# Performance work log

Hardware: AMD Instinct MI355X
Metric: run time of the kernel (lower is better)

Reference implementation:

```python
import jax, jax.numpy as jnp
import numpy as np

N = 50000   # nodes
E = 1600000 # edges
D = 128     # feature dim (in = hidden = 128)


def setup_inputs() -> dict:
    key = jax.random.key(0)
    k1, k2, k3, k4 = jax.random.split(key, 4)
    scale = 1.0 / np.sqrt(D)
    return {
        "x": jax.random.normal(k1, (N, D), jnp.float32),
        "edge_index": jax.random.randint(k2, (2, E), 0, N, dtype=jnp.int32),
        "W0": jax.random.normal(k3, (D, D), jnp.float32) * scale,
        "b0": jnp.zeros((D,), jnp.float32),
        "W1": jax.random.normal(k4, (D, D), jnp.float32) * scale,
        "b1": jnp.zeros((D,), jnp.float32),
    }


def _gcn_norm(edge_index, num_nodes):
    # Add self-loops, compute symmetric normalization D^-1/2 A_hat D^-1/2.
    loop = jnp.arange(num_nodes, dtype=edge_index.dtype)
    src = jnp.concatenate([edge_index[0], loop])
    dst = jnp.concatenate([edge_index[1], loop])
    deg = jax.ops.segment_sum(jnp.ones_like(dst, jnp.float32), dst,
                              num_segments=num_nodes)
    dinv = jnp.where(deg > 0, jax.lax.rsqrt(deg), 0.0)
    norm = dinv[dst] * dinv[src]  # [E+N]
    return src, dst, norm


def _gcn_layer(x, src, dst, norm, W, b, num_nodes):
    h = x @ W                                  # [N, D]
    msg = h[src] * norm[:, None]               # gather + scale  [E+N, D]
    out = jax.ops.segment_sum(msg, dst, num_segments=num_nodes)  # scatter-add
    return out + b


def reference(x, edge_index, W0, b0, W1, b1):
    num_nodes = x.shape[0]
    src, dst, norm = _gcn_norm(edge_index, num_nodes)
    # forward loops over the first k=2 convs, ReLU after each (as in source)
    x = jax.nn.relu(_gcn_layer(x, src, dst, norm, W0, b0, num_nodes))
    x = jax.nn.relu(_gcn_layer(x, src, dst, norm, W1, b1, num_nodes))
    return x
```

## Files before the change

kernel.cpp:

```cpp
#include <hip/hip_runtime.h>
#include <hip/hip_bf16.h>

#define D 128
#define CHUNK 8192


typedef __attribute__((ext_vector_type(8))) short short8;
typedef __attribute__((ext_vector_type(4))) float floatx4;

static __device__ inline unsigned int f2bf(float f) {
    unsigned int u = __float_as_uint(f);
    return (u + 0x7FFFu + ((u >> 16) & 1u)) >> 16;
}
static __device__ inline float bflo(unsigned int u) { return __uint_as_float(u << 16); }
static __device__ inline float bfhi(unsigned int u) { return __uint_as_float(u & 0xFFFF0000u); }

__global__ __launch_bounds__(256) void k01_swz_hist(const float* __restrict__ W0,
                                                    const float* __restrict__ W1,
                                                    short8* __restrict__ whi0, short8* __restrict__ wlo0,
                                                    short8* __restrict__ whi1, short8* __restrict__ wlo1,
                                                    const int* __restrict__ dst,
                                                    int* __restrict__ blockhist, int E_) {
    __shared__ int h[256];
    const int tid = threadIdx.x;
    if (blockIdx.x < 16) {
        int gid = blockIdx.x * 256 + tid;
        const float* W = (gid < 2048) ? W0 : W1;
        short8* whi = (gid < 2048) ? whi0 : whi1;
        short8* wlo = (gid < 2048) ? wlo0 : wlo1;
        int t2 = gid & 2047;
        int t = t2 >> 8, q = (t2 >> 6) & 3, lane = t2 & 63;
        short8 hi, lo;
        #pragma unroll
        for (int j = 0; j < 8; ++j) {
            int k = q * 32 + (lane >> 4) * 8 + j;
            int n = t * 16 + (lane & 15);
            float w = W[k * D + n];
            unsigned int hh = f2bf(w);
            hi[j] = (short)hh;
            lo[j] = (short)f2bf(w - __uint_as_float(hh << 16));
        }
        whi[t2] = hi;
        wlo[t2] = lo;
    } else {
        const int b = blockIdx.x - 16;
        h[tid] = 0;
        __syncthreads();
        const int e0 = b * CHUNK;
        const int e1 = min(E_, e0 + CHUNK);
        for (int e = e0 + tid; e < e1; e += 256)
            atomicAdd(&h[dst[e] >> 8], 1);
        __syncthreads();
        blockhist[b * 256 + tid] = h[tid];
    }
}

__global__ __launch_bounds__(256) void k2_scan(const int* __restrict__ blockhist,
                                               int* __restrict__ gbase,
                                               int* __restrict__ bucket_offs,
                                               int NB, int NBUK, int E_) {
    __shared__ int s[256];
    const int myb = blockIdx.x, tid = threadIdx.x;
    int total = 0, prefix = 0;
    #pragma unroll 4
    for (int b2 = 0; b2 < NB; ++b2) {
        int t = blockhist[b2 * 256 + tid];
        total += t;
        prefix += (b2 < myb) ? t : 0;
    }
    s[tid] = total;
    __syncthreads();
    #pragma unroll
    for (int off = 1; off < 256; off <<= 1) {
        int x = (tid >= off) ? s[tid - off] : 0;
        __syncthreads();
        s[tid] += x;
        __syncthreads();
    }
    int bstart = s[tid] - total;
    gbase[myb * 256 + tid] = bstart + prefix;
    if (myb == 0) {
        if (tid < NBUK) bucket_offs[tid] = bstart;
        if (tid == 0) bucket_offs[NBUK] = E_;
    }
}

__global__ __launch_bounds__(256) void k3_scatter(const int* __restrict__ dst,
                                                  const int* __restrict__ src,
                                                  const int* __restrict__ gbase,
                                                  unsigned int* __restrict__ buf, int E_) {
    __shared__ int c[256];
    const int b = blockIdx.x, tid = threadIdx.x;
    c[tid] = gbase[b * 256 + tid];
    __syncthreads();
    const int e0 = b * CHUNK;
    const int e1 = min(E_, e0 + CHUNK);
    for (int e = e0 + tid; e < e1; e += 256) {
        int v = dst[e];
        int sdx = src[e];
        int pos = atomicAdd(&c[v >> 8], 1);
        buf[pos] = (unsigned int)sdx | ((unsigned int)(v & 255) << 16);
    }
}

__global__ __launch_bounds__(256) void k4_bucket(const unsigned int* __restrict__ buf,
                                                 const int* __restrict__ bucket_offs,
                                                 int* __restrict__ offs,
                                                 float* __restrict__ dinv,
                                                 int* __restrict__ col, int N_, int E_) {
    __shared__ int h[256];
    __shared__ int s[256];
    __shared__ int c[256];
    const int beta = blockIdx.x, tid = threadIdx.x;
    const int start = bucket_offs[beta];
    const int end   = bucket_offs[beta + 1];

    h[tid] = 0;
    __syncthreads();
    for (int e = start + tid; e < end; e += 256)
        atomicAdd(&h[(buf[e] >> 16) & 255], 1);
    __syncthreads();

    int deg = h[tid];
    s[tid] = deg;
    __syncthreads();
    #pragma unroll
    for (int off = 1; off < 256; off <<= 1) {
        int x = (tid >= off) ? s[tid - off] : 0;
        __syncthreads();
        s[tid] += x;
        __syncthreads();
    }
    int excl = s[tid] - deg;

    int v0 = beta * 256 + tid;
    if (v0 < N_) {
        offs[v0] = start + excl;
        dinv[v0] = rsqrtf((float)(deg + 1));
    }
    if (beta == 0 && tid == 0) offs[N_] = E_;
    c[tid] = start + excl;
    __syncthreads();

    for (int e = start + tid; e < end; e += 256) {
        unsigned int p = buf[e];
        int pos = atomicAdd(&c[(p >> 16) & 255], 1);
        col[pos] = (int)(p & 0xFFFFu);
    }
}

__global__ __launch_bounds__(256) void gemm_mfma(const float* __restrict__ A,
                                                 const short8* __restrict__ whi,
                                                 const short8* __restrict__ wlo,
                                                 const float* __restrict__ dinv,
                                                 unsigned int* __restrict__ Gu, int nrows) {
    __shared__ float tileT[128][65];

    const int tid  = threadIdx.x;
    const int wave = tid >> 6, lane = tid & 63;
    const int m = lane & 15, quad = lane >> 4;
    const int rowInBlk = wave * 16;
    const int arow = min(blockIdx.x * 64 + rowInBlk + m, nrows - 1);
    const float* Ap = A + (size_t)arow * D + quad * 8;

    floatx4 acc[8];
    #pragma unroll
    for (int t = 0; t < 8; ++t) acc[t] = (floatx4){0.f, 0.f, 0.f, 0.f};

    #pragma unroll
    for (int q = 0; q < 4; ++q) {
        float4 a0 = *(const float4*)(Ap + q * 32);
        float4 a1 = *(const float4*)(Ap + q * 32 + 4);
        float av[8] = {a0.x, a0.y, a0.z, a0.w, a1.x, a1.y, a1.z, a1.w};
        short8 ahi, alo;
        #pragma unroll
        for (int j = 0; j < 8; ++j) {
            unsigned int h = f2bf(av[j]);
            ahi[j] = (short)h;
            alo[j] = (short)f2bf(av[j] - __uint_as_float(h << 16));
        }
        #pragma unroll
        for (int t = 0; t < 8; ++t) {
            short8 bh = whi[(t * 4 + q) * 64 + lane];
            short8 bl = wlo[(t * 4 + q) * 64 + lane];
            acc[t] = __builtin_amdgcn_mfma_f32_16x16x32_bf16(ahi, bh, acc[t], 0, 0, 0);
            acc[t] = __builtin_amdgcn_mfma_f32_16x16x32_bf16(alo, bh, acc[t], 0, 0, 0);
            acc[t] = __builtin_amdgcn_mfma_f32_16x16x32_bf16(ahi, bl, acc[t], 0, 0, 0);
        }
    }

    #pragma unroll
    for (int t = 0; t < 8; ++t)
        #pragma unroll
        for (int r = 0; r < 4; ++r)
            tileT[t * 16 + m][rowInBlk + quad * 4 + r] = acc[t][r];
    __syncthreads();

    const int orow = tid >> 2, seg = tid & 3;
    const int grow = blockIdx.x * 64 + orow;
    if (grow < nrows) {
        float s = dinv[grow];
        const int p = seg >> 1;
        unsigned int* Gp = Gu + ((size_t)(p * nrows + grow)) * 32 + (seg & 1) * 16;
        #pragma unroll
        for (int i = 0; i < 4; ++i) {
            int c0 = seg * 32 + i * 8;
            uint4 o4;
            o4.x = f2bf(tileT[c0 + 0][orow] * s) | (f2bf(tileT[c0 + 1][orow] * s) << 16);
            o4.y = f2bf(tileT[c0 + 2][orow] * s) | (f2bf(tileT[c0 + 3][orow] * s) << 16);
            o4.z = f2bf(tileT[c0 + 4][orow] * s) | (f2bf(tileT[c0 + 5][orow] * s) << 16);
            o4.w = f2bf(tileT[c0 + 6][orow] * s) | (f2bf(tileT[c0 + 7][orow] * s) << 16);
            ((uint4*)Gp)[i] = o4;
        }
    }
}

__global__ __launch_bounds__(256) void aggregate_kernel(const unsigned int* __restrict__ Gu,
                                                        const int* __restrict__ offs,
                                                        const int* __restrict__ col,
                                                        const float* __restrict__ dinv,
                                                        const float* __restrict__ bias,
                                                        float* __restrict__ out, int nnodes,
                                                        int ngroups) {
    const int bid  = blockIdx.x;
    const int xcd  = bid & 7;
    const int plane = xcd >> 2;
    const int i    = (bid >> 3) * 4 + (xcd & 3);
    if (i >= ngroups) return;
    const int lane = threadIdx.x & 31;
    const int node = i * 8 + (threadIdx.x >> 5);
    if (node >= nnodes) return;
    const unsigned int* P = Gu + (size_t)plane * nnodes * 32;

    unsigned int su = P[(size_t)node * 32 + lane];
    float ax = bflo(su), ay = bfhi(su);

    int s = offs[node];
    int e = offs[node + 1];
    int idx = s;
    for (; idx + 8 <= e; idx += 8) {
        int j0 = col[idx + 0], j1 = col[idx + 1], j2 = col[idx + 2], j3 = col[idx + 3];
        int j4 = col[idx + 4], j5 = col[idx + 5], j6 = col[idx + 6], j7 = col[idx + 7];
        unsigned int u0 = P[(size_t)j0 * 32 + lane];
        unsigned int u1 = P[(size_t)j1 * 32 + lane];
        unsigned int u2 = P[(size_t)j2 * 32 + lane];
        unsigned int u3 = P[(size_t)j3 * 32 + lane];
        unsigned int u4 = P[(size_t)j4 * 32 + lane];
        unsigned int u5 = P[(size_t)j5 * 32 + lane];
        unsigned int u6 = P[(size_t)j6 * 32 + lane];
        unsigned int u7 = P[(size_t)j7 * 32 + lane];
        ax += ((bflo(u0) + bflo(u1)) + (bflo(u2) + bflo(u3))) +
              ((bflo(u4) + bflo(u5)) + (bflo(u6) + bflo(u7)));
        ay += ((bfhi(u0) + bfhi(u1)) + (bfhi(u2) + bfhi(u3))) +
              ((bfhi(u4) + bfhi(u5)) + (bfhi(u6) + bfhi(u7)));
    }
    for (; idx + 4 <= e; idx += 4) {
        int j0 = col[idx + 0], j1 = col[idx + 1], j2 = col[idx + 2], j3 = col[idx + 3];
        unsigned int u0 = P[(size_t)j0 * 32 + lane];
        unsigned int u1 = P[(size_t)j1 * 32 + lane];
        unsigned int u2 = P[(size_t)j2 * 32 + lane];
        unsigned int u3 = P[(size_t)j3 * 32 + lane];
        ax += (bflo(u0) + bflo(u1)) + (bflo(u2) + bflo(u3));
        ay += (bfhi(u0) + bfhi(u1)) + (bfhi(u2) + bfhi(u3));
    }
    for (; idx < e; ++idx) {
        unsigned int u = P[(size_t)col[idx] * 32 + lane];
        ax += bflo(u);
        ay += bfhi(u);
    }

    float dv = dinv[node];
    float2 bb = ((const float2*)bias)[plane * 32 + lane];
    float2 o;
    o.x = fmaxf(fmaf(dv, ax, bb.x), 0.f);
    o.y = fmaxf(fmaf(dv, ay, bb.y), 0.f);
    ((float2*)out)[(size_t)node * 64 + plane * 32 + lane] = o;
}

extern "C" void kernel_launch(void* const* d_in, const int* in_sizes, int n_in,
                              void* d_out, int out_size, void* d_ws, size_t ws_size,
                              hipStream_t stream) {
    const float* x    = (const float*)d_in[0];
    const int*   edge = (const int*)d_in[1];
    const float* W0   = (const float*)d_in[2];
    const float* b0   = (const float*)d_in[3];
    const float* W1   = (const float*)d_in[4];
    const float* b1   = (const float*)d_in[5];
    float* out = (float*)d_out;

    const int N_ = in_sizes[0] / D;
    const int E_ = in_sizes[1] / 2;
    const int* srcp = edge;
    const int* dstp = edge + E_;

    const int NB   = (E_ + CHUNK - 1) / CHUNK;
    const int NBUK = (N_ + 255) >> 8;

    char* p = (char*)d_ws;
    auto carve = [&](size_t bytes) { char* q = p; p += (bytes + 255) & ~(size_t)255; return q; };
    int*          blockhist = (int*)          carve((size_t)NB * 256 * 4);
    int*          gbase     = (int*)          carve((size_t)NB * 256 * 4);
    int*          buck_offs = (int*)          carve((size_t)(NBUK + 1) * 4);
    int*          offs      = (int*)          carve((size_t)(N_ + 1) * 4);
    float*        dinv      = (float*)        carve((size_t)N_ * 4);
    unsigned int* buf       = (unsigned int*) carve((size_t)E_ * 4);
    int*          col       = (int*)          carve((size_t)E_ * 4);
    unsigned int* gu        = (unsigned int*) carve((size_t)N_ * 64 * 4);
    short8*       whi0      = (short8*)       carve(2048 * 16);
    short8*       wlo0      = (short8*)       carve(2048 * 16);
    short8*       whi1      = (short8*)       carve(2048 * 16);
    short8*       wlo1      = (short8*)       carve(2048 * 16);

    k01_swz_hist<<<16 + NB, 256, 0, stream>>>(W0, W1, whi0, wlo0, whi1, wlo1,
                                              dstp, blockhist, E_);
    k2_scan     <<<NB,      256, 0, stream>>>(blockhist, gbase, buck_offs, NB, NBUK, E_);
    k3_scatter  <<<NB,      256, 0, stream>>>(dstp, srcp, gbase, buf, E_);
    k4_bucket   <<<NBUK,    256, 0, stream>>>(buf, buck_offs, offs, dinv, col, N_, E_);

    const int gmb = (N_ + 63) / 64;
    const int ngroups = (N_ + 7) / 8;
    const int agrid   = ((ngroups + 3) / 4) * 8;

    gemm_mfma       <<<gmb,   256, 0, stream>>>(x, whi0, wlo0, dinv, gu, N_);
    aggregate_kernel<<<agrid, 256, 0, stream>>>(gu, offs, col, dinv, b0, out, N_, ngroups);
    gemm_mfma       <<<gmb,   256, 0, stream>>>(out, whi1, wlo1, dinv, gu, N_);
    aggregate_kernel<<<agrid, 256, 0, stream>>>(gu, offs, col, dinv, b1, out, N_, ngroups);
}
```

Before: 269.1 us.

## Fuse scan into scatter kernel and stage neighbor indices in LDS for aggregation

Merges the per-block prefix scan and the bucket scatter into one kernel. This drops a launch and the gbase round-trip through global memory. The aggregation kernel now loads each 8-node group's offsets and column indices into shared memory cooperatively, with a global-memory fallback when the span exceeds the capacity. This replaces scattered per-lane index loads with LDS reads, at the cost of extra barriers and shared memory per block.

```diff
diff --git a/kernel.cpp b/kernel.cpp
--- a/kernel.cpp
+++ b/kernel.cpp
@@ -3,6 +3,7 @@
 
 #define D 128
 #define CHUNK 8192
+#define SPAN_CAP 768
 
 
 typedef __attribute__((ext_vector_type(8))) short short8;
@@ -55,11 +56,14 @@
     }
 }
 
-__global__ __launch_bounds__(256) void k2_scan(const int* __restrict__ blockhist,
-                                               int* __restrict__ gbase,
-                                               int* __restrict__ bucket_offs,
-                                               int NB, int NBUK, int E_) {
+__global__ __launch_bounds__(256) void k23_scan_scatter(const int* __restrict__ blockhist,
+                                                        const int* __restrict__ dst,
+                                                        const int* __restrict__ src,
+                                                        int* __restrict__ bucket_offs,
+                                                        unsigned int* __restrict__ buf,
+                                                        int NB, int NBUK, int E_) {
     __shared__ int s[256];
+    __shared__ int c[256];
     const int myb = blockIdx.x, tid = threadIdx.x;
     int total = 0, prefix = 0;
     #pragma unroll 4
@@ -78,22 +82,14 @@
         __syncthreads();
     }
     int bstart = s[tid] - total;
-    gbase[myb * 256 + tid] = bstart + prefix;
     if (myb == 0) {
         if (tid < NBUK) bucket_offs[tid] = bstart;
         if (tid == 0) bucket_offs[NBUK] = E_;
     }
-}
-
-__global__ __launch_bounds__(256) void k3_scatter(const int* __restrict__ dst,
-                                                  const int* __restrict__ src,
-                                                  const int* __restrict__ gbase,
-                                                  unsigned int* __restrict__ buf, int E_) {
-    __shared__ int c[256];
-    const int b = blockIdx.x, tid = threadIdx.x;
-    c[tid] = gbase[b * 256 + tid];
-    __syncthreads();
-    const int e0 = b * CHUNK;
+    c[tid] = bstart + prefix;
+    __syncthreads();
+
+    const int e0 = myb * CHUNK;
     const int e1 = min(E_, e0 + CHUNK);
     for (int e = e0 + tid; e < e1; e += 256) {
         int v = dst[e];
@@ -222,51 +218,87 @@
                                                         const float* __restrict__ bias,
                                                         float* __restrict__ out, int nnodes,
                                                         int ngroups) {
-    const int bid  = blockIdx.x;
-    const int xcd  = bid & 7;
+    __shared__ int scol[SPAN_CAP];
+    __shared__ int soffs[9];
+    const int bid   = blockIdx.x;
+    const int xcd   = bid & 7;
     const int plane = xcd >> 2;
-    const int i    = (bid >> 3) * 4 + (xcd & 3);
+    const int i     = (bid >> 3) * 4 + (xcd & 3);
     if (i >= ngroups) return;
-    const int lane = threadIdx.x & 31;
-    const int node = i * 8 + (threadIdx.x >> 5);
+    const int tid   = threadIdx.x;
+    const int node0 = i * 8;
+
+    if (tid < 9) soffs[tid] = offs[min(node0 + tid, nnodes)];
+    __syncthreads();
+    const int s0   = soffs[0];
+    const int span = soffs[8] - s0;
+    const bool lds_ok = (span <= SPAN_CAP);
+    if (lds_ok) {
+        for (int k = tid; k < span; k += 256) scol[k] = col[s0 + k];
+    }
+    __syncthreads();
+
+    const int lane = tid & 31;
+    const int node = node0 + (tid >> 5);
     if (node >= nnodes) return;
     const unsigned int* P = Gu + (size_t)plane * nnodes * 32;
 
     unsigned int su = P[(size_t)node * 32 + lane];
     float ax = bflo(su), ay = bfhi(su);
 
-    int s = offs[node];
-    int e = offs[node + 1];
+    const int s = soffs[tid >> 5];
+    const int e = soffs[(tid >> 5) + 1];
     int idx = s;
-    for (; idx + 8 <= e; idx += 8) {
-        int j0 = col[idx + 0], j1 = col[idx + 1], j2 = col[idx + 2], j3 = col[idx + 3];
-        int j4 = col[idx + 4], j5 = col[idx + 5], j6 = col[idx + 6], j7 = col[idx + 7];
-        unsigned int u0 = P[(size_t)j0 * 32 + lane];
-        unsigned int u1 = P[(size_t)j1 * 32 + lane];
-        unsigned int u2 = P[(size_t)j2 * 32 + lane];
-        unsigned int u3 = P[(size_t)j3 * 32 + lane];
-        unsigned int u4 = P[(size_t)j4 * 32 + lane];
-        unsigned int u5 = P[(size_t)j5 * 32 + lane];
-        unsigned int u6 = P[(size_t)j6 * 32 + lane];
-        unsigned int u7 = P[(size_t)j7 * 32 + lane];
-        ax += ((bflo(u0) + bflo(u1)) + (bflo(u2) + bflo(u3))) +
-              ((bflo(u4) + bflo(u5)) + (bflo(u6) + bflo(u7)));
-        ay += ((bfhi(u0) + bfhi(u1)) + (bfhi(u2) + bfhi(u3))) +
-              ((bfhi(u4) + bfhi(u5)) + (bfhi(u6) + bfhi(u7)));
-    }
-    for (; idx + 4 <= e; idx += 4) {
-        int j0 = col[idx + 0], j1 = col[idx + 1], j2 = col[idx + 2], j3 = col[idx + 3];
-        unsigned int u0 = P[(size_t)j0 * 32 + lane];
-        unsigned int u1 = P[(size_t)j1 * 32 + lane];
-        unsigned int u2 = P[(size_t)j2 * 32 + lane];
-        unsigned int u3 = P[(size_t)j3 * 32 + lane];
-        ax += (bflo(u0) + bflo(u1)) + (bflo(u2) + bflo(u3));
-        ay += (bfhi(u0) + bfhi(u1)) + (bfhi(u2) + bfhi(u3));
-    }
-    for (; idx < e; ++idx) {
-        unsigned int u = P[(size_t)col[idx] * 32 + lane];
-        ax += bflo(u);
-        ay += bfhi(u);
+
+    if (lds_ok) {
+        const int b0 = s - s0;
+        int k = 0;
+        const int deg = e - s;
+        for (; k + 8 <= deg; k += 8) {
+            int j0 = scol[b0 + k + 0], j1 = scol[b0 + k + 1], j2 = scol[b0 + k + 2], j3 = scol[b0 + k + 3];
+            int j4 = scol[b0 + k + 4], j5 = scol[b0 + k + 5], j6 = scol[b0 + k + 6], j7 = scol[b0 + k + 7];
+            unsigned int u0 = P[(size_t)j0 * 32 + lane];
+            unsigned int u1 = P[(size_t)j1 * 32 + lane];
+            unsigned int u2 = P[(size_t)j2 * 32 + lane];
+            unsigned int u3 = P[(size_t)j3 * 32 + lane];
+            unsigned int u4 = P[(size_t)j4 * 32 + lane];
+            unsigned int u5 = P[(size_t)j5 * 32 + lane];
+            unsigned int u6 = P[(size_t)j6 * 32 + lane];
+            unsigned int u7 = P[(size_t)j7 * 32 + lane];
+            ax += ((bflo(u0) + bflo(u1)) + (bflo(u2) + bflo(u3))) +
+                  ((bflo(u4) + bflo(u5)) + (bflo(u6) + bflo(u7)));
+            ay += ((bfhi(u0) + bfhi(u1)) + (bfhi(u2) + bfhi(u3))) +
+                  ((bfhi(u4) + bfhi(u5)) + (bfhi(u6) + bfhi(u7)));
+        }
+        for (; k + 4 <= deg; k += 4) {
+            int j0 = scol[b0 + k + 0], j1 = scol[b0 + k + 1], j2 = scol[b0 + k + 2], j3 = scol[b0 + k + 3];
+            unsigned int u0 = P[(size_t)j0 * 32 + lane];
+            unsigned int u1 = P[(size_t)j1 * 32 + lane];
+            unsigned int u2 = P[(size_t)j2 * 32 + lane];
+            unsigned int u3 = P[(size_t)j3 * 32 + lane];
+            ax += (bflo(u0) + bflo(u1)) + (bflo(u2) + bflo(u3));
+            ay += (bfhi(u0) + bfhi(u1)) + (bfhi(u2) + bfhi(u3));
+        }
+        for (; k < deg; ++k) {
+            unsigned int u = P[(size_t)scol[b0 + k] * 32 + lane];
+            ax += bflo(u);
+            ay += bfhi(u);
+        }
+    } else {
+        for (; idx + 4 <= e; idx += 4) {
+            int j0 = col[idx + 0], j1 = col[idx + 1], j2 = col[idx + 2], j3 = col[idx + 3];
+            unsigned int u0 = P[(size_t)j0 * 32 + lane];
+            unsigned int u1 = P[(size_t)j1 * 32 + lane];
+            unsigned int u2 = P[(size_t)j2 * 32 + lane];
+            unsigned int u3 = P[(size_t)j3 * 32 + lane];
+            ax += (bflo(u0) + bflo(u1)) + (bflo(u2) + bflo(u3));
+            ay += (bfhi(u0) + bfhi(u1)) + (bfhi(u2) + bfhi(u3));
+        }
+        for (; idx < e; ++idx) {
+            unsigned int u = P[(size_t)col[idx] * 32 + lane];
+            ax += bflo(u);
+            ay += bfhi(u);
+        }
     }
 
     float dv = dinv[node];
@@ -299,7 +331,6 @@
     char* p = (char*)d_ws;
     auto carve = [&](size_t bytes) { char* q = p; p += (bytes + 255) & ~(size_t)255; return q; };
     int*          blockhist = (int*)          carve((size_t)NB * 256 * 4);
-    int*          gbase     = (int*)          carve((size_t)NB * 256 * 4);
     int*          buck_offs = (int*)          carve((size_t)(NBUK + 1) * 4);
     int*          offs      = (int*)          carve((size_t)(N_ + 1) * 4);
     float*        dinv      = (float*)        carve((size_t)N_ * 4);
@@ -311,11 +342,11 @@
     short8*       whi1      = (short8*)       carve(2048 * 16);
     short8*       wlo1      = (short8*)       carve(2048 * 16);
 
-    k01_swz_hist<<<16 + NB, 256, 0, stream>>>(W0, W1, whi0, wlo0, whi1, wlo1,
-                                              dstp, blockhist, E_);
-    k2_scan     <<<NB,      256, 0, stream>>>(blockhist, gbase, buck_offs, NB, NBUK, E_);
-    k3_scatter  <<<NB,      256, 0, stream>>>(dstp, srcp, gbase, buf, E_);
-    k4_bucket   <<<NBUK,    256, 0, stream>>>(buf, buck_offs, offs, dinv, col, N_, E_);
+    k01_swz_hist   <<<16 + NB, 256, 0, stream>>>(W0, W1, whi0, wlo0, whi1, wlo1,
+                                                 dstp, blockhist, E_);
+    k23_scan_scatter<<<NB,     256, 0, stream>>>(blockhist, dstp, srcp, buck_offs, buf,
+                                                 NB, NBUK, E_);
+    k4_bucket      <<<NBUK,    256, 0, stream>>>(buf, buck_offs, offs, dinv, col, N_, E_);
 
     const int gmb = (N_ + 63) / 64;
     const int ngroups = (N_ + 7) / 8;
```

After: 259.1 us. -3.7%, faster.
